# Kernel optimization log

Hardware: AMD Instinct MI355X
Metric: run time of the kernel (lower is better)

## Reference

```python
import jax, jax.numpy as jnp
import numpy as np
from jax import lax

EMB = 200   # embedding_dim (GRU hidden size)
SD = 12     # state_dim
AD = 4      # action_dim
CD = 8      # context_dim
LCD = 6     # local_context_dim
T = 100     # rollout steps
BS = 2048   # batch size
EPS = 0.01 ** 2


def _lin(x, w, b):
    # torch nn.Linear convention: y = x @ W^T + b
    return x @ w.T + b


def setup_inputs() -> dict:
    key = jax.random.key(0)
    ks = iter(jax.random.split(key, 64))

    def p(shape):
        return jax.random.normal(next(ks), shape, jnp.float32) * 0.05

    d = {}
    d["x"] = jax.random.normal(next(ks), (BS, SD), jnp.float32)
    d["u"] = jax.random.normal(next(ks), (T, BS, AD), jnp.float32)
    d["ctx_mean"] = jax.random.normal(next(ks), (BS, CD), jnp.float32)
    d["local_ctx"] = jax.random.normal(next(ks), (T, BS, LCD), jnp.float32)
    # state_embed_net: Lin(SD,200) ReLU, Lin(200,EMB) Tanh
    d["se_w1"], d["se_b1"] = p((200, SD)), p((200,))
    d["se_w2"], d["se_b2"] = p((EMB, 200)), p((EMB,))
    # action_embed_net: Lin(AD,200) ReLU, Lin(200,EMB) ReLU
    d["ae_w1"], d["ae_b1"] = p((200, AD)), p((200,))
    d["ae_w2"], d["ae_b2"] = p((EMB, 200)), p((EMB,))
    # context_embed_net: Lin(CD,200) ReLU, Lin(200,EMB) ReLU
    d["ce_w1"], d["ce_b1"] = p((200, CD)), p((200,))
    d["ce_w2"], d["ce_b2"] = p((EMB, 200)), p((EMB,))
    # local_context_embed_net: Lin(LCD,200) ReLU, Lin(200,EMB) ReLU
    d["lce_w1"], d["lce_b1"] = p((200, LCD)), p((200,))
    d["lce_w2"], d["lce_b2"] = p((EMB, 200)), p((EMB,))
    # decode_net: Lin(EMB,200) ReLU, Lin(200,SD)
    d["dec_w1"], d["dec_b1"] = p((200, EMB)), p((200,))
    d["dec_w2"], d["dec_b2"] = p((SD, 200)), p((SD,))
    # GRUCell(input=3*EMB, hidden=EMB)
    d["gru_wih"], d["gru_bih"] = p((3 * EMB, 3 * EMB)), p((3 * EMB,))
    d["gru_whh"], d["gru_bhh"] = p((3 * EMB, EMB)), p((3 * EMB,))
    # hidden_cov_net: Lin(EMB,200) ReLU, Lin(200,SD)
    d["cov_w1"], d["cov_b1"] = p((200, EMB)), p((200,))
    d["cov_w2"], d["cov_b2"] = p((SD, 200)), p((SD,))
    return d


def _forward(x, u, ctx_mean, local_ctx,
             se_w1, se_b1, se_w2, se_b2,
             ae_w1, ae_b1, ae_w2, ae_b2,
             ce_w1, ce_b1, ce_w2, ce_b2,
             lce_w1, lce_b1, lce_w2, lce_b2,
             dec_w1, dec_b1, dec_w2, dec_b2,
             gru_wih, gru_bih, gru_whh, gru_bhh,
             cov_w1, cov_b1, cov_w2, cov_b2):
    relu = jax.nn.relu
    # embeddings (vectorized over all timesteps at once)
    state_embed = jnp.tanh(_lin(relu(_lin(x, se_w1, se_b1)), se_w2, se_b2))          # [BS, EMB]
    action_embed_all = relu(_lin(relu(_lin(u, ae_w1, ae_b1)), ae_w2, ae_b2))         # [T, BS, EMB]
    ctx_embed = relu(_lin(relu(_lin(ctx_mean, ce_w1, ce_b1)), ce_w2, ce_b2))         # [BS, EMB]
    lce_all = relu(_lin(relu(_lin(local_ctx, lce_w1, lce_b1)), lce_w2, lce_b2))      # [T, BS, EMB]

    def step(h, inp):
        a, lc = inp
        gru_in = jnp.concatenate([ctx_embed, a, lc], axis=-1)   # [BS, 3*EMB]
        gi = gru_in @ gru_wih.T + gru_bih                        # [BS, 3*EMB]
        gh = h @ gru_whh.T + gru_bhh                             # [BS, 3*EMB]
        ir, iz, inn = jnp.split(gi, 3, axis=-1)
        hr, hz, hn = jnp.split(gh, 3, axis=-1)
        r = jax.nn.sigmoid(ir + hr)
        z = jax.nn.sigmoid(iz + hz)
        n = jnp.tanh(inn + r * hn)
        h_new = (1.0 - z) * n + z * h
        return h_new, h_new

    _, hs = lax.scan(step, state_embed, (action_embed_all, lce_all))
    hiddens = jnp.concatenate([state_embed[None], hs], axis=0)   # [T+1, BS, EMB]

    state_mean = _lin(relu(_lin(hiddens, dec_w1, dec_b1)), dec_w2, dec_b2)           # [T+1, BS, SD]
    cov = jax.nn.softplus(_lin(relu(_lin(hiddens, cov_w1, cov_b1)), cov_w2, cov_b2)) + EPS
    state_std = jnp.sqrt(cov)                                                        # [T+1, BS, SD]
    return state_mean, state_std


def reference(x, u, ctx_mean, local_ctx,
              se_w1, se_b1, se_w2, se_b2,
              ae_w1, ae_b1, ae_w2, ae_b2,
              ce_w1, ce_b1, ce_w2, ce_b2,
              lce_w1, lce_b1, lce_w2, lce_b2,
              dec_w1, dec_b1, dec_w2, dec_b2,
              gru_wih, gru_bih, gru_whh, gru_bhh,
              cov_w1, cov_b1, cov_w2, cov_b2):
    return _forward(x, u, ctx_mean, local_ctx,
                    se_w1, se_b1, se_w2, se_b2,
                    ae_w1, ae_b1, ae_w2, ae_b2,
                    ce_w1, ce_b1, ce_w2, ce_b2,
                    lce_w1, lce_b1, lce_w2, lce_b2,
                    dec_w1, dec_b1, dec_w2, dec_b2,
                    gru_wih, gru_bih, gru_whh, gru_bhh,
                    cov_w1, cov_b1, cov_w2, cov_b2)
```

## Files before the change

kernel.cpp:

```cpp
#include <hip/hip_runtime.h>
#include <math.h>

#define TT   100
#define BSZ  2048
#define NCH  4
#define CT   (TT/NCH)
#define CR   (CT*BSZ)
#define DR   ((TT+1)*BSZ)
#define NG   624
#define GO   208
#define EPSV 1e-4f

typedef short bfrag __attribute__((ext_vector_type(8)));
typedef float facc  __attribute__((ext_vector_type(4)));

static __device__ __forceinline__ short f2b(float x){
  union { float f; unsigned u; } c; c.f = x;
  unsigned r = (c.u + 0x7FFFu + ((c.u >> 16) & 1u)) >> 16;
  return (short)r;
}
static __device__ __forceinline__ float b2f(short s){
  union { unsigned u; float f; } c; c.u = ((unsigned)(unsigned short)s) << 16;
  return c.f;
}
static __device__ __forceinline__ facc mfma16(bfrag a, bfrag b, facc c){
  return __builtin_amdgcn_mfma_f32_16x16x32_bf16(a, b, c, 0, 0, 0);
}
static __device__ __forceinline__ float sigm(float x){ return 1.f/(1.f+__expf(-x)); }
static __device__ __forceinline__ float tanh_f(float x){
  x = fminf(fmaxf(x, -15.f), 15.f);
  float e = __expf(2.f*x);
  return (e-1.f)/(e+1.f);
}
static __device__ __forceinline__ void bar_lgkm(){
  asm volatile("s_waitcnt lgkmcnt(0)\n\ts_barrier" ::: "memory");
}

__global__ __launch_bounds__(256) void k_prep(
    const float* __restrict__ ae_w2, const float* __restrict__ lce_w2,
    const float* __restrict__ dec_w1, const float* __restrict__ cov_w1,
    const float* __restrict__ dec_w2, const float* __restrict__ cov_w2,
    const float* __restrict__ wih, const float* __restrict__ whh,
    const float* __restrict__ se_w2, const float* __restrict__ ce_w2,
    const float* __restrict__ ae_b2, const float* __restrict__ lce_b2,
    const float* __restrict__ dec_b1, const float* __restrict__ cov_b1,
    const float* __restrict__ dec_b2, const float* __restrict__ cov_b2,
    const float* __restrict__ bhh,
    const float* __restrict__ ae_w1, const float* __restrict__ ae_b1,
    const float* __restrict__ lce_w1, const float* __restrict__ lce_b1,
    short* __restrict__ aew2b, short* __restrict__ lcew2b,
    short* __restrict__ decw1b, short* __restrict__ covw1b,
    short* __restrict__ decw2b, short* __restrict__ covw2b,
    short* __restrict__ wihab, short* __restrict__ wihlb, short* __restrict__ whhb,
    float* __restrict__ sew2T, float* __restrict__ cew2T, float* __restrict__ wihcT,
    float* __restrict__ aeb2p, float* __restrict__ lceb2p,
    float* __restrict__ decb1p, float* __restrict__ covb1p,
    float* __restrict__ decb2p, float* __restrict__ covb2p,
    float* __restrict__ bhhp,
    short* __restrict__ aw1b, short* __restrict__ lw1b,
    float* __restrict__ aeb1p, float* __restrict__ lceb1p){
  int job = blockIdx.y;
  int idx = blockIdx.x*256 + threadIdx.x;
  if (job < 4){
    if (idx >= 208*224) return;
    const float* s = (job==0)?ae_w2:(job==1)?lce_w2:(job==2)?dec_w1:cov_w1;
    short* d = (job==0)?aew2b:(job==1)?lcew2b:(job==2)?decw1b:covw1b;
    int n = idx / 224, k = idx - n*224;
    d[idx] = f2b((n < 200 && k < 200) ? s[n*200 + k] : 0.f);
  } else if (job < 6){
    if (idx >= 16*224) return;
    const float* s = (job==4)?dec_w2:cov_w2;
    short* d = (job==4)?decw2b:covw2b;
    int n = idx / 224, k = idx - n*224;
    d[idx] = f2b((n < 12 && k < 200) ? s[n*200 + k] : 0.f);
  } else if (job < 8){
    if (idx >= NG*224) return;
    int colOff = (job==6) ? 200 : 400;
    short* d = (job==6)?wihab:wihlb;
    int n = idx / 224, k = idx - n*224;
    int gate = n / GO, o = n - gate*GO;
    d[idx] = f2b((o < 200 && k < 200) ? wih[(size_t)(gate*200+o)*600 + colOff + k] : 0.f);
  } else if (job == 8){
    if (idx >= NG*224) return;
    int n = idx / 224, k = idx - n*224;
    int gate = n / GO, o = n - gate*GO;
    whhb[idx] = f2b((o < 200 && k < 200) ? whh[(size_t)(gate*200+o)*200 + k] : 0.f);
  } else if (job < 11){
    if (idx >= 200*200) return;
    const float* s = (job==9)?se_w2:ce_w2;
    float* d = (job==9)?sew2T:cew2T;
    int k = idx / 200, n = idx - k*200;
    d[idx] = s[n*200 + k];
  } else if (job == 11){
    if (idx >= 200*600) return;
    int k = idx / 600, n = idx - k*600;
    wihcT[idx] = wih[(size_t)n*600 + k];
  } else if (job == 12){
    if (idx < 208)       aeb2p[idx]      = (idx < 200) ? ae_b2[idx] : 0.f;
    else if (idx < 416)  lceb2p[idx-208] = (idx-208 < 200) ? lce_b2[idx-208] : 0.f;
    else if (idx < 624)  decb1p[idx-416] = (idx-416 < 200) ? dec_b1[idx-416] : 0.f;
    else if (idx < 832)  covb1p[idx-624] = (idx-624 < 200) ? cov_b1[idx-624] : 0.f;
    else if (idx < 848)  decb2p[idx-832] = (idx-832 < 12) ? dec_b2[idx-832] : 0.f;
    else if (idx < 864)  covb2p[idx-848] = (idx-848 < 12) ? cov_b2[idx-848] : 0.f;
    else if (idx < 864+NG){
      int n = idx - 864, gate = n / GO, o = n - gate*GO;
      bhhp[n] = (o < 200) ? bhh[gate*200 + o] : 0.f;
    }
  } else {
    if (idx < 208*32){
      int n = idx >> 5, k = idx & 31;
      aw1b[idx] = f2b((n < 200 && k < 4) ? ae_w1[n*4 + k] : 0.f);
      lw1b[idx] = f2b((n < 200 && k < 6) ? lce_w1[n*6 + k] : 0.f);
    } else if (idx < 208*32 + 208){
      int n = idx - 208*32;
      aeb1p[n]  = (n < 200) ? ae_b1[n] : 0.f;
      lceb1p[n] = (n < 200) ? lce_b1[n] : 0.f;
    }
  }
}

__global__ __launch_bounds__(256) void k_zero(short* __restrict__ hidb, float* __restrict__ hcar){
  int idx = blockIdx.x*256 + threadIdx.x;
  if (idx < CR*24){
    int row = idx / 24, k = 200 + (idx - row*24);
    hidb[((size_t)BSZ + row)*224 + k] = 0;
  } else if (idx < CR*24 + BSZ*24){
    int j = idx - CR*24;
    int row = j / 24, k = 200 + (j - row*24);
    hcar[(size_t)row*224 + k] = 0.f;
  }
}

__global__ __launch_bounds__(256) void k_mlp2(const float* __restrict__ x, int Kin,
    const float* __restrict__ w1, const float* __restrict__ b1,
    const float* __restrict__ w2T, const float* __restrict__ b2,
    int act_tanh,
    float* __restrict__ outf, int outf_stride,
    short* __restrict__ outb){
  int row = blockIdx.x, t = threadIdx.x;
  __shared__ float xr[16];
  __shared__ float h1[200];
  if (t < Kin) xr[t] = x[(size_t)row*Kin + t];
  __syncthreads();
  if (t < 200){
    float a = b1[t];
    #pragma unroll 4
    for (int i = 0; i < Kin; ++i) a += xr[i] * w1[t*Kin + i];
    h1[t] = fmaxf(a, 0.f);
  }
  __syncthreads();
  if (t < 224){
    float v = 0.f;
    if (t < 200){
      float a = b2[t];
      #pragma unroll 4
      for (int k = 0; k < 200; ++k) a += h1[k] * w2T[k*200 + t];
      v = act_tanh ? tanh_f(a) : fmaxf(a, 0.f);
    }
    if (t < outf_stride) outf[(size_t)row*outf_stride + t] = v;
    if (outb) outb[(size_t)row*224 + t] = f2b(v);
  }
}

__global__ __launch_bounds__(256) void k_gictx(const float* __restrict__ ctxe,
    const float* __restrict__ wT, const float* __restrict__ bih, float* __restrict__ gic){
  int b = blockIdx.x, t = threadIdx.x;
  __shared__ float cr[200];
  if (t < 200) cr[t] = ctxe[(size_t)b*200 + t];
  __syncthreads();
  for (int n = t; n < NG; n += 256){
    int gate = n / GO, o = n - gate*GO;
    float a = 0.f;
    if (o < 200){
      int sc = gate*200 + o;
      a = bih[sc];
      #pragma unroll 4
      for (int k = 0; k < 200; ++k) a += cr[k] * wT[k*600 + sc];
    }
    gic[(size_t)b*NG + n] = a;
  }
}

__global__ __launch_bounds__(256, 2) void k_fuse(
    const float* __restrict__ u, const float* __restrict__ lc,
    const short* __restrict__ aw1b, const float* __restrict__ aeb1p,
    const short* __restrict__ lw1b, const float* __restrict__ lceb1p,
    const short* __restrict__ aw2b, const float* __restrict__ ab2p,
    const short* __restrict__ lw2b, const float* __restrict__ lb2p,
    const short* __restrict__ wihab, const short* __restrict__ wihlb,
    short* __restrict__ gibuf, int rowBase){
  __shared__ short t1[2][64][232];
  __shared__ short uB[64][40];
  __shared__ short lcB[64][40];
  int tid = threadIdx.x;
  int r0 = blockIdx.x * 64;
  for (int e = tid; e < 2560; e += 256){
    int row = e / 40, k = e - row*40;
    size_t rg = (size_t)rowBase + r0 + row;
    uB[row][k]  = (k < 4) ? f2b(u[rg*4 + k])  : 0;
    lcB[row][k] = (k < 6) ? f2b(lc[rg*6 + k]) : 0;
  }
  for (int e = tid; e < 2*64*16; e += 256){
    int c = e & 15, row = (e >> 4) & 63, ch = e >> 10;
    t1[ch][row][208 + c] = 0;
  }
  bar_lgkm();
  int w = tid >> 6, lane = tid & 63, lm = lane & 15, lq = lane >> 4;
  int ch = w >> 1;
  int mb = (w & 1) * 2;
  {
    const short (*src)[40] = ch ? lcB : uB;
    const short* w1b = ch ? lw1b : aw1b;
    const float* b1p = ch ? lceb1p : aeb1p;
    bfrag Au0 = *reinterpret_cast<const bfrag*>(&src[mb*16 + lm][lq*8]);
    bfrag Au1 = *reinterpret_cast<const bfrag*>(&src[(mb+1)*16 + lm][lq*8]);
    for (int nt = 0; nt < 13; ++nt){
      int col = nt*16 + lm;
      bfrag Bf = *reinterpret_cast<const bfrag*>(&w1b[col*32 + lq*8]);
      facc z = {0.f,0.f,0.f,0.f};
      facc a0 = mfma16(Au0, Bf, z);
      facc a1 = mfma16(Au1, Bf, z);
      float bias = b1p[col];
      #pragma unroll
      for (int i = 0; i < 4; ++i){
        t1[ch][mb*16     + lq*4 + i][col] = f2b(fmaxf(a0[i] + bias, 0.f));
        t1[ch][(mb+1)*16 + lq*4 + i][col] = f2b(fmaxf(a1[i] + bias, 0.f));
      }
    }
  }
  bar_lgkm();
  {
    const short* w2b = ch ? lw2b : aw2b;
    const float* b2p = ch ? lb2p : ab2p;
    bfrag A0[7], A1[7];
    #pragma unroll
    for (int ks = 0; ks < 7; ++ks){
      A0[ks] = *reinterpret_cast<const bfrag*>(&t1[ch][mb*16 + lm][ks*32 + lq*8]);
      A1[ks] = *reinterpret_cast<const bfrag*>(&t1[ch][(mb+1)*16 + lm][ks*32 + lq*8]);
    }
    bfrag Bc[7], Bn[7];
    #pragma unroll
    for (int ks = 0; ks < 7; ++ks)
      Bc[ks] = *reinterpret_cast<const bfrag*>(&w2b[(size_t)lm*224 + ks*32 + lq*8]);
    for (int nt = 0; nt < 13; ++nt){
      int col = nt*16 + lm;
      if (nt < 12){
        int coln = col + 16;
        #pragma unroll
        for (int ks = 0; ks < 7; ++ks)
          Bn[ks] = *reinterpret_cast<const bfrag*>(&w2b[(size_t)coln*224 + ks*32 + lq*8]);
      }
      facc a0 = {0.f,0.f,0.f,0.f}, a1 = {0.f,0.f,0.f,0.f};
      #pragma unroll
      for (int ks = 0; ks < 7; ++ks){
        a0 = mfma16(A0[ks], Bc[ks], a0);
        a1 = mfma16(A1[ks], Bc[ks], a1);
      }
      float bias = b2p[col];
      #pragma unroll
      for (int i = 0; i < 4; ++i){
        t1[ch][mb*16     + lq*4 + i][col] = f2b(fmaxf(a0[i] + bias, 0.f));
        t1[ch][(mb+1)*16 + lq*4 + i][col] = f2b(fmaxf(a1[i] + bias, 0.f));
      }
      #pragma unroll
      for (int ks = 0; ks < 7; ++ks) Bc[ks] = Bn[ks];
    }
  }
  int ntS = (w >> 1) ? 20 : 0;
  int ntE = (w >> 1) ? 39 : 20;
  bfrag Bc4[14];
  {
    int col = ntS*16 + lm;
    #pragma unroll
    for (int ks = 0; ks < 7; ++ks){
      Bc4[ks]   = *reinterpret_cast<const bfrag*>(&wihab[(size_t)col*224 + ks*32 + lq*8]);
      Bc4[7+ks] = *reinterpret_cast<const bfrag*>(&wihlb[(size_t)col*224 + ks*32 + lq*8]);
    }
  }
  bar_lgkm();
  {
    bfrag Am[2][14];
    #pragma unroll
    for (int m2 = 0; m2 < 2; ++m2)
      #pragma unroll
      for (int ks = 0; ks < 7; ++ks){
        Am[m2][ks]   = *reinterpret_cast<const bfrag*>(&t1[0][(mb+m2)*16 + lm][ks*32 + lq*8]);
        Am[m2][7+ks] = *reinterpret_cast<const bfrag*>(&t1[1][(mb+m2)*16 + lm][ks*32 + lq*8]);
      }
    for (int nt = ntS; nt < ntE; ++nt){
      int col = nt*16 + lm;
      bfrag Bn4[14];
      if (nt + 1 < ntE){
        int coln = col + 16;
        #pragma unroll
        for (int ks = 0; ks < 7; ++ks){
          Bn4[ks]   = *reinterpret_cast<const bfrag*>(&wihab[(size_t)coln*224 + ks*32 + lq*8]);
          Bn4[7+ks] = *reinterpret_cast<const bfrag*>(&wihlb[(size_t)coln*224 + ks*32 + lq*8]);
        }
      }
      facc a0 = {0.f,0.f,0.f,0.f}, a1 = {0.f,0.f,0.f,0.f};
      #pragma unroll
      for (int kk = 0; kk < 14; ++kk){
        a0 = mfma16(Am[0][kk], Bc4[kk], a0);
        a1 = mfma16(Am[1][kk], Bc4[kk], a1);
      }
      #pragma unroll
      for (int i = 0; i < 4; ++i){
        int rl0 = mb*16 + lq*4 + i;
        gibuf[((size_t)r0 + rl0)*NG + col]      = f2b(a0[i]);
        gibuf[((size_t)r0 + rl0 + 16)*NG + col] = f2b(a1[i]);
      }
      #pragma unroll
      for (int kk = 0; kk < 14; ++kk) Bc4[kk] = Bn4[kk];
    }
  }
}

__global__ __launch_bounds__(512, 2) void k_gru4(
    const short* __restrict__ gib, const float* __restrict__ gic,
    const float* __restrict__ hin,
    const short* __restrict__ whhb, const float* __restrict__ bhhp,
    short* __restrict__ hidb, float* __restrict__ hout){
  __shared__ float ghT[624][12];
  __shared__ short hB[2][16][232];
  int tid = threadIdx.x;
  int r0 = blockIdx.x * 8;
  int w = tid >> 6, lane = tid & 63, lm = lane & 15, lq = lane >> 4;
  int nt0 = w*5;
  int cnt = (w < 7) ? 5 : 4;
  bfrag Bg[5][7];
  float bia[5];
  #pragma unroll
  for (int s = 0; s < 5; ++s) if (s < cnt){
    int col = (nt0+s)*16 + lm;
    bia[s] = bhhp[col];
    #pragma unroll
    for (int ks = 0; ks < 7; ++ks)
      Bg[s][ks] = *reinterpret_cast<const bfrag*>(&whhb[(size_t)col*224 + ks*32 + lq*8]);
  }
  int gj = tid >> 1, grh = tid & 1;
  bool gact = (tid < 416) && (gj < 200);
  float hreg[4], gicv[3][4];
  #pragma unroll
  for (int i = 0; i < 4; ++i){
    hreg[i] = gact ? hin[(size_t)(r0 + grh*4 + i)*224 + gj] : 0.f;
    #pragma unroll
    for (int g = 0; g < 3; ++g)
      gicv[g][i] = gact ? gic[(size_t)(r0 + grh*4 + i)*NG + g*GO + gj] : 0.f;
  }
  for (int e = tid; e < 2*16*232; e += 512) (&hB[0][0][0])[e] = 0;
  __syncthreads();
  for (int e = tid; e < 8*224; e += 512){
    int row = e / 224, k = e - row*224;
    hB[0][row][k] = f2b(hin[(size_t)(r0+row)*224 + k]);
  }
  __syncthreads();
  for (int t = 0; t < CT; ++t){
    int cur = t & 1, nxt = cur ^ 1;
    float gr[4], gz[4], gn[4];
    const short* gp = gib + ((size_t)t*BSZ + r0 + grh*4)*NG + gj;
    #pragma unroll
    for (int i = 0; i < 4; ++i){
      gr[i] = gact ? b2f(gp[i*NG        ]) + gicv[0][i] : 0.f;
      gz[i] = gact ? b2f(gp[i*NG + GO   ]) + gicv[1][i] : 0.f;
      gn[i] = gact ? b2f(gp[i*NG + 2*GO ]) + gicv[2][i] : 0.f;
    }
    bfrag hf[7];
    #pragma unroll
    for (int ks = 0; ks < 7; ++ks)
      hf[ks] = *reinterpret_cast<const bfrag*>(&hB[cur][lm][ks*32 + lq*8]);
    #pragma unroll
    for (int s = 0; s < 5; ++s) if (s < cnt){
      facc a = {0.f,0.f,0.f,0.f};
      #pragma unroll
      for (int ks = 0; ks < 7; ++ks) a = mfma16(hf[ks], Bg[s][ks], a);
      if (lq < 2){
        int col = (nt0+s)*16 + lm;
        a[0] += bia[s]; a[1] += bia[s]; a[2] += bia[s]; a[3] += bia[s];
        *reinterpret_cast<facc*>(&ghT[col][lq*4]) = a;
      }
    }
    bar_lgkm();
    if (gact){
      facc R = *reinterpret_cast<facc*>(&ghT[gj][grh*4]);
      facc Z = *reinterpret_cast<facc*>(&ghT[GO + gj][grh*4]);
      facc N = *reinterpret_cast<facc*>(&ghT[2*GO + gj][grh*4]);
      short* hp = hidb + ((size_t)(t+1)*BSZ + r0 + grh*4)*224 + gj;
      #pragma unroll
      for (int i = 0; i < 4; ++i){
        float r  = sigm(gr[i] + R[i]);
        float zz = sigm(gz[i] + Z[i]);
        float n  = tanh_f(gn[i] + r*N[i]);
        float hn = (1.f - zz)*n + zz*hreg[i];
        hreg[i] = hn;
        short hb = f2b(hn);
        hB[nxt][grh*4 + i][gj] = hb;
        hp[i*224] = hb;
      }
    }
    bar_lgkm();
  }
  if (gact)
    #pragma unroll
    for (int i = 0; i < 4; ++i)
      hout[(size_t)(r0 + grh*4 + i)*224 + gj] = hreg[i];
}

__global__ __launch_bounds__(256) void k_dec(
    const short* __restrict__ hidb, int rowStart, int outBase,
    const short* __restrict__ dw1b, const float* __restrict__ db1p,
    const short* __restrict__ dw2b, const float* __restrict__ db2p,
    const short* __restrict__ cw1b, const float* __restrict__ cb1p,
    const short* __restrict__ cw2b, const float* __restrict__ cb2p,
    float* __restrict__ outMean, float* __restrict__ outStd){
  __shared__ short h1t[64][224];
  int tid = threadIdx.x;
  int r0 = rowStart + blockIdx.x * 64;
  int w = tid >> 6, lane = tid & 63, lm = lane & 15, lq = lane >> 4;
  for (int e = tid; e < 64*16; e += 256)
    h1t[e >> 4][208 + (e & 15)] = 0;
  bfrag hf[4][7];
  #pragma unroll
  for (int m = 0; m < 4; ++m)
    #pragma unroll
    for (int ks = 0; ks < 7; ++ks)
      hf[m][ks] = *reinterpret_cast<const bfrag*>(&hidb[(size_t)(r0 + m*16 + lm)*224 + ks*32 + lq*8]);
  int ntStart = (w == 0) ? 0 : 4 + 3*(w-1);
  int ntCnt   = (w == 0) ? 4 : 3;
  for (int pass = 0; pass < 2; ++pass){
    const short* w1b = pass ? cw1b : dw1b;
    const float* b1p = pass ? cb1p : db1p;
    const short* w2b = pass ? cw2b : dw2b;
    const float* b2p = pass ? cb2p : db2p;
    bar_lgkm();
    for (int nti = 0; nti < ntCnt; ++nti){
      int nt = ntStart + nti;
      int col = nt*16 + lm;
      facc z = {0.f,0.f,0.f,0.f};
      facc acc[4] = {z,z,z,z};
      #pragma unroll
      for (int ks = 0; ks < 7; ++ks){
        bfrag bf = *reinterpret_cast<const bfrag*>(&w1b[(size_t)col*224 + ks*32 + lq*8]);
        #pragma unroll
        for (int m = 0; m < 4; ++m) acc[m] = mfma16(hf[m][ks], bf, acc[m]);
      }
      float bias = b1p[col];
      #pragma unroll
      for (int m = 0; m < 4; ++m)
        #pragma unroll
        for (int i = 0; i < 4; ++i)
          h1t[m*16 + lq*4 + i][col] = f2b(fmaxf(acc[m][i] + bias, 0.f));
    }
    bar_lgkm();
    bfrag a2[7];
    #pragma unroll
    for (int ks = 0; ks < 7; ++ks)
      a2[ks] = *reinterpret_cast<const bfrag*>(&h1t[w*16 + lm][ks*32 + lq*8]);
    facc acc = {0.f,0.f,0.f,0.f};
    #pragma unroll
    for (int ks = 0; ks < 7; ++ks){
      bfrag bf = *reinterpret_cast<const bfrag*>(&w2b[(size_t)lm*224 + ks*32 + lq*8]);
      acc = mfma16(a2[ks], bf, acc);
    }
    if (lm < 12){
      float bias = b2p[lm];
      #pragma unroll
      for (int i = 0; i < 4; ++i){
        size_t rg = (size_t)outBase + r0 + w*16 + lq*4 + i;
        float v = acc[i] + bias;
        if (pass){
          float sp = (v > 15.f) ? v : log1pf(__expf(v));
          outStd[rg*12 + lm] = sqrtf(sp + EPSV);
        } else {
          outMean[rg*12 + lm] = v;
        }
      }
    }
  }
}

extern "C" void kernel_launch(void* const* d_in, const int* in_sizes, int n_in,
                              void* d_out, int out_size, void* d_ws, size_t ws_size,
                              hipStream_t stream){
  (void)in_sizes; (void)n_in; (void)out_size; (void)ws_size;
  const float* x      = (const float*)d_in[0];
  const float* u      = (const float*)d_in[1];
  const float* ctxm   = (const float*)d_in[2];
  const float* lctx   = (const float*)d_in[3];
  const float* se_w1  = (const float*)d_in[4];
  const float* se_b1  = (const float*)d_in[5];
  const float* se_w2  = (const float*)d_in[6];
  const float* se_b2  = (const float*)d_in[7];
  const float* ae_w1  = (const float*)d_in[8];
  const float* ae_b1  = (const float*)d_in[9];
  const float* ae_w2  = (const float*)d_in[10];
  const float* ae_b2  = (const float*)d_in[11];
  const float* ce_w1  = (const float*)d_in[12];
  const float* ce_b1  = (const float*)d_in[13];
  const float* ce_w2  = (const float*)d_in[14];
  const float* ce_b2  = (const float*)d_in[15];
  const float* lce_w1 = (const float*)d_in[16];
  const float* lce_b1 = (const float*)d_in[17];
  const float* lce_w2 = (const float*)d_in[18];
  const float* lce_b2 = (const float*)d_in[19];
  const float* dec_w1 = (const float*)d_in[20];
  const float* dec_b1 = (const float*)d_in[21];
  const float* dec_w2 = (const float*)d_in[22];
  const float* dec_b2 = (const float*)d_in[23];
  const float* wih    = (const float*)d_in[24];
  const float* bih    = (const float*)d_in[25];
  const float* whh    = (const float*)d_in[26];
  const float* bhh    = (const float*)d_in[27];
  const float* cov_w1 = (const float*)d_in[28];
  const float* cov_b1 = (const float*)d_in[29];
  const float* cov_w2 = (const float*)d_in[30];
  const float* cov_b2 = (const float*)d_in[31];

  char* ws = (char*)d_ws;
  size_t off = 0;
  auto alloc = [&](size_t sz) -> char* {
    char* p = ws + off; off = (off + sz + 255) & ~(size_t)255; return p;
  };
  short* aew2b  = (short*)alloc(208*224*2);
  short* lcew2b = (short*)alloc(208*224*2);
  short* decw1b = (short*)alloc(208*224*2);
  short* covw1b = (short*)alloc(208*224*2);
  short* decw2b = (short*)alloc(16*224*2);
  short* covw2b = (short*)alloc(16*224*2);
  short* wihab  = (short*)alloc((size_t)NG*224*2);
  short* wihlb  = (short*)alloc((size_t)NG*224*2);
  short* whhb   = (short*)alloc((size_t)NG*224*2);
  float* sew2T  = (float*)alloc(200*200*4);
  float* cew2T  = (float*)alloc(200*200*4);
  float* wihcT  = (float*)alloc(200*600*4);
  float* aeb2p  = (float*)alloc(208*4);
  float* lceb2p = (float*)alloc(208*4);
  float* decb1p = (float*)alloc(208*4);
  float* covb1p = (float*)alloc(208*4);
  float* decb2p = (float*)alloc(16*4);
  float* covb2p = (float*)alloc(16*4);
  float* bhhp   = (float*)alloc(NG*4);
  short* aw1b   = (short*)alloc(208*32*2);
  short* lw1b   = (short*)alloc(208*32*2);
  float* aeb1p  = (float*)alloc(208*4);
  float* lceb1p = (float*)alloc(208*4);
  float* gic    = (float*)alloc((size_t)BSZ*NG*4);
  float* h0f    = (float*)alloc((size_t)BSZ*224*4);
  float* hcar   = (float*)alloc((size_t)BSZ*224*4);
  float* ctxef  = (float*)alloc((size_t)BSZ*200*4);
  short* hidbuf = (short*)alloc((size_t)(CT+1)*BSZ*224*2);
  short* gibuf  = (short*)alloc((size_t)CR*NG*2);

  float* outMean = (float*)d_out;
  float* outStd  = outMean + (size_t)DR*12;

  k_prep<<<dim3((NG*224 + 255)/256, 14), 256, 0, stream>>>(
      ae_w2, lce_w2, dec_w1, cov_w1, dec_w2, cov_w2, wih, whh, se_w2, ce_w2,
      ae_b2, lce_b2, dec_b1, cov_b1, dec_b2, cov_b2, bhh,
      ae_w1, ae_b1, lce_w1, lce_b1,
      aew2b, lcew2b, decw1b, covw1b, decw2b, covw2b,
      wihab, wihlb, whhb, sew2T, cew2T, wihcT,
      aeb2p, lceb2p, decb1p, covb1p, decb2p, covb2p, bhhp,
      aw1b, lw1b, aeb1p, lceb1p);
  k_zero<<<(CR*24 + BSZ*24 + 255)/256, 256, 0, stream>>>(hidbuf, hcar);

  k_mlp2<<<BSZ, 256, 0, stream>>>(x,    12, se_w1, se_b1, sew2T, se_b2, 1, h0f,   224, hidbuf);
  k_mlp2<<<BSZ, 256, 0, stream>>>(ctxm,  8, ce_w1, ce_b1, cew2T, ce_b2, 0, ctxef, 200, (short*)nullptr);
  k_gictx<<<BSZ, 256, 0, stream>>>(ctxef, wihcT, bih, gic);

  for (int c = 0; c < NCH; ++c){
    k_fuse<<<CR/64, 256, 0, stream>>>(u, lctx, aw1b, aeb1p, lw1b, lceb1p,
                                      aew2b, aeb2p, lcew2b, lceb2p,
                                      wihab, wihlb, gibuf, c*CR);
    k_gru4<<<BSZ/8, 512, 0, stream>>>(gibuf, gic, (c == 0) ? h0f : hcar,
                                      whhb, bhhp, hidbuf, hcar);
    int rowStart = (c == 0) ? 0 : BSZ;
    int nRows    = (c == 0) ? (CT+1)*BSZ : CT*BSZ;
    k_dec<<<nRows/64, 256, 0, stream>>>(hidbuf, rowStart, c*CT*BSZ,
                                        decw1b, decb1p, decw2b, decb2p,
                                        covw1b, covb1p, covw2b, covb2p,
                                        outMean, outStd);
  }
}
```

Measured before the change: 1.302 ms.

## Enlarge k_fuse tile to 128 rows and reuse resident W_ih across row blocks

k_fuse now runs 512 threads on 128-row tiles. Each of 8 waves owns a fixed slice of about 5 output column tiles and keeps two column tiles of W_ih B-fragments in registers, iterating over all 8 row blocks with A fragments reloaded from LDS. This reuses each W_ih fragment loaded from global across 128 rows instead of 32, cutting weight traffic. The cost is more LDS use per block, repeated A-fragment LDS reads, and a higher register load that may lower occupancy.

```diff
diff --git a/kernel.cpp b/kernel.cpp
--- a/kernel.cpp
+++ b/kernel.cpp
@@ -181,7 +181,7 @@
   }
 }
 
-__global__ __launch_bounds__(256, 2) void k_fuse(
+__global__ __launch_bounds__(512, 2) void k_fuse(
     const float* __restrict__ u, const float* __restrict__ lc,
     const short* __restrict__ aw1b, const float* __restrict__ aeb1p,
     const short* __restrict__ lw1b, const float* __restrict__ lceb1p,
@@ -189,25 +189,25 @@
     const short* __restrict__ lw2b, const float* __restrict__ lb2p,
     const short* __restrict__ wihab, const short* __restrict__ wihlb,
     short* __restrict__ gibuf, int rowBase){
-  __shared__ short t1[2][64][232];
-  __shared__ short uB[64][40];
-  __shared__ short lcB[64][40];
+  __shared__ short t1[2][128][232];
+  __shared__ short uB[128][40];
+  __shared__ short lcB[128][40];
   int tid = threadIdx.x;
-  int r0 = blockIdx.x * 64;
-  for (int e = tid; e < 2560; e += 256){
+  int r0 = blockIdx.x * 128;
+  for (int e = tid; e < 128*40; e += 512){
     int row = e / 40, k = e - row*40;
     size_t rg = (size_t)rowBase + r0 + row;
     uB[row][k]  = (k < 4) ? f2b(u[rg*4 + k])  : 0;
     lcB[row][k] = (k < 6) ? f2b(lc[rg*6 + k]) : 0;
   }
-  for (int e = tid; e < 2*64*16; e += 256){
-    int c = e & 15, row = (e >> 4) & 63, ch = e >> 10;
+  for (int e = tid; e < 2*128*16; e += 512){
+    int c = e & 15, row = (e >> 4) & 127, ch = e >> 11;
     t1[ch][row][208 + c] = 0;
   }
   bar_lgkm();
   int w = tid >> 6, lane = tid & 63, lm = lane & 15, lq = lane >> 4;
-  int ch = w >> 1;
-  int mb = (w & 1) * 2;
+  int ch = w >> 2;
+  int mb = (w & 3) * 2;
   {
     const short (*src)[40] = ch ? lcB : uB;
     const short* w1b = ch ? lw1b : aw1b;
@@ -266,52 +266,42 @@
       for (int ks = 0; ks < 7; ++ks) Bc[ks] = Bn[ks];
     }
   }
-  int ntS = (w >> 1) ? 20 : 0;
-  int ntE = (w >> 1) ? 39 : 20;
-  bfrag Bc4[14];
-  {
-    int col = ntS*16 + lm;
-    #pragma unroll
-    for (int ks = 0; ks < 7; ++ks){
-      Bc4[ks]   = *reinterpret_cast<const bfrag*>(&wihab[(size_t)col*224 + ks*32 + lq*8]);
-      Bc4[7+ks] = *reinterpret_cast<const bfrag*>(&wihlb[(size_t)col*224 + ks*32 + lq*8]);
-    }
-  }
   bar_lgkm();
   {
-    bfrag Am[2][14];
-    #pragma unroll
-    for (int m2 = 0; m2 < 2; ++m2)
-      #pragma unroll
-      for (int ks = 0; ks < 7; ++ks){
-        Am[m2][ks]   = *reinterpret_cast<const bfrag*>(&t1[0][(mb+m2)*16 + lm][ks*32 + lq*8]);
-        Am[m2][7+ks] = *reinterpret_cast<const bfrag*>(&t1[1][(mb+m2)*16 + lm][ks*32 + lq*8]);
-      }
-    for (int nt = ntS; nt < ntE; ++nt){
-      int col = nt*16 + lm;
-      bfrag Bn4[14];
-      if (nt + 1 < ntE){
-        int coln = col + 16;
+    int ntBase = w*5;
+    int ntCnt  = (w < 7) ? 5 : 4;
+    for (int gs = 0; gs < ntCnt; gs += 2){
+      int gc = ntCnt - gs; if (gc > 2) gc = 2;
+      bfrag Bres[2][14];
+      #pragma unroll
+      for (int s = 0; s < 2; ++s) if (s < gc){
+        int col = (ntBase + gs + s)*16 + lm;
         #pragma unroll
         for (int ks = 0; ks < 7; ++ks){
-          Bn4[ks]   = *reinterpret_cast<const bfrag*>(&wihab[(size_t)coln*224 + ks*32 + lq*8]);
-          Bn4[7+ks] = *reinterpret_cast<const bfrag*>(&wihlb[(size_t)coln*224 + ks*32 + lq*8]);
+          Bres[s][ks]   = *reinterpret_cast<const bfrag*>(&wihab[(size_t)col*224 + ks*32 + lq*8]);
+          Bres[s][7+ks] = *reinterpret_cast<const bfrag*>(&wihlb[(size_t)col*224 + ks*32 + lq*8]);
         }
       }
-      facc a0 = {0.f,0.f,0.f,0.f}, a1 = {0.f,0.f,0.f,0.f};
-      #pragma unroll
-      for (int kk = 0; kk < 14; ++kk){
-        a0 = mfma16(Am[0][kk], Bc4[kk], a0);
-        a1 = mfma16(Am[1][kk], Bc4[kk], a1);
-      }
-      #pragma unroll
-      for (int i = 0; i < 4; ++i){
-        int rl0 = mb*16 + lq*4 + i;
-        gibuf[((size_t)r0 + rl0)*NG + col]      = f2b(a0[i]);
-        gibuf[((size_t)r0 + rl0 + 16)*NG + col] = f2b(a1[i]);
-      }
-      #pragma unroll
-      for (int kk = 0; kk < 14; ++kk) Bc4[kk] = Bn4[kk];
+      for (int m = 0; m < 8; ++m){
+        bfrag Af[14];
+        #pragma unroll
+        for (int ks = 0; ks < 7; ++ks){
+          Af[ks]   = *reinterpret_cast<const bfrag*>(&t1[0][m*16 + lm][ks*32 + lq*8]);
+          Af[7+ks] = *reinterpret_cast<const bfrag*>(&t1[1][m*16 + lm][ks*32 + lq*8]);
+        }
+        #pragma unroll
+        for (int s = 0; s < 2; ++s) if (s < gc){
+          facc a = {0.f,0.f,0.f,0.f};
+          #pragma unroll
+          for (int kk = 0; kk < 14; ++kk) a = mfma16(Af[kk], Bres[s][kk], a);
+          int col = (ntBase + gs + s)*16 + lm;
+          #pragma unroll
+          for (int i = 0; i < 4; ++i){
+            int rl = m*16 + lq*4 + i;
+            gibuf[((size_t)r0 + rl)*NG + col] = f2b(a[i]);
+          }
+        }
+      }
     }
   }
 }
@@ -569,9 +559,9 @@
   k_gictx<<<BSZ, 256, 0, stream>>>(ctxef, wihcT, bih, gic);
 
   for (int c = 0; c < NCH; ++c){
-    k_fuse<<<CR/64, 256, 0, stream>>>(u, lctx, aw1b, aeb1p, lw1b, lceb1p,
-                                      aew2b, aeb2p, lcew2b, lceb2p,
-                                      wihab, wihlb, gibuf, c*CR);
+    k_fuse<<<CR/128, 512, 0, stream>>>(u, lctx, aw1b, aeb1p, lw1b, lceb1p,
+                                       aew2b, aeb2p, lcew2b, lceb2p,
+                                       wihab, wihlb, gibuf, c*CR);
     k_gru4<<<BSZ/8, 512, 0, stream>>>(gibuf, gic, (c == 0) ? h0f : hcar,
                                       whhb, bhhp, hidbuf, hcar);
     int rowStart = (c == 0) ? 0 : BSZ;
```

Result: faster. 1.188 ms (-8.8%).
